# Performance work log

Measured on AMD Instinct MI355X. Metric: run time of the kernel, lower is better.

## Reference

```python
import jax, jax.numpy as jnp
import numpy as np

# ---- dims from init_kwargs ----
CB, DB = 2, 256
IN_DIM = CB + DB            # control_bits + data_bits
OUT_UNITS = DB              # output_units = data_bits
STATE_UNITS = 512           # hidden_state_dim
NUM_HEADS = 2
NUM_SHIFT = 3
M = 64                      # memory content size (word length)
B, S = 16, 512
N_ADDR = S                  # memory_addresses_size == -1 -> seq_len

# per-head interface parameter layout: shift(s), jd, jump(3), gamma, erase, add, key, beta, gate
SPLITS = [NUM_SHIFT, 1, 3, 1, M, M, M, 1, 1]
OFFS = np.cumsum([0] + SPLITS).tolist()
UPD_PER_HEAD = OFFS[-1]
READ_SIZE = NUM_HEADS * M
UPDATE_SIZE = NUM_HEADS * UPD_PER_HEAD
CTRL_IN = IN_DIM + STATE_UNITS + READ_SIZE
EPS = 1e-12


def setup_inputs() -> dict:
    key = jax.random.key(0)
    ks = jax.random.split(key, 4)
    sc = 1.0 / np.sqrt(CTRL_IN)
    return {
        "inputs": jax.random.normal(ks[0], (B, S, IN_DIM), jnp.float32),
        "W_s": jax.random.normal(ks[1], (CTRL_IN, STATE_UNITS), jnp.float32) * sc,
        "b_s": jnp.zeros((STATE_UNITS,), jnp.float32),
        "W_o": jax.random.normal(ks[2], (CTRL_IN, OUT_UNITS), jnp.float32) * sc,
        "b_o": jnp.zeros((OUT_UNITS,), jnp.float32),
        "W_u": jax.random.normal(ks[3], (CTRL_IN, UPDATE_SIZE), jnp.float32) * sc,
        "b_u": jnp.zeros((UPDATE_SIZE,), jnp.float32),
    }


def _cell(carry, x_t, W_s, b_s, W_o, b_o, W_u, b_u):
    state, wt, wt_dyn, mem = carry          # [B,St], [B,H,N], [B,H,N], [B,M,N]
    # --- read from memory with previous head attention ---
    read = jnp.einsum('bhn,bmn->bhm', wt, mem).reshape(B, READ_SIZE)
    # --- controller (single-layer RNN producing output / state / interface params) ---
    comb = jnp.concatenate([x_t, state, read], axis=-1)
    new_state = jax.nn.sigmoid(comb @ W_s + b_s)
    out = jax.nn.sigmoid(comb @ W_o + b_o)
    upd = (comb @ W_u + b_u).reshape(B, NUM_HEADS, UPD_PER_HEAD)
    s_raw, jd, j, gamma, erase, add, k, beta, g = [
        upd[..., OFFS[i]:OFFS[i + 1]] for i in range(len(SPLITS))]
    s = jax.nn.softmax(jax.nn.softplus(s_raw), axis=-1)     # [B,H,SHIFT]
    jd = jax.nn.sigmoid(jd)                                 # [B,H,1]
    j = jax.nn.softmax(j, axis=-1)                          # [B,H,3]
    gamma = 1.0 + jax.nn.softplus(gamma)                    # [B,H,1]
    erase = jax.nn.sigmoid(erase)                           # [B,H,M]
    beta = jax.nn.softplus(beta)                            # [B,H,1]
    g = jax.nn.sigmoid(g)                                   # [B,H,1]
    # --- bookmark (dynamic snapshot) update ---
    wt_dyn_new = (1.0 - jd) * wt_dyn + jd * wt
    wt_fixed = jnp.zeros((1, 1, N_ADDR), mem.dtype).at[..., 0].set(1.0)
    # --- jump between current head / dynamic bookmark / fixed address 0 ---
    w = j[..., 0:1] * wt + j[..., 1:2] * wt_dyn_new + j[..., 2:3] * wt_fixed
    # --- content addressing (is_cam=True): cosine sim key vs memory columns ---
    kn = k / (jnp.linalg.norm(k, axis=-1, keepdims=True) + EPS)
    mn = mem / (jnp.linalg.norm(mem, axis=1, keepdims=True) + EPS)
    wt_k = jax.nn.softmax(beta * jnp.einsum('bhm,bmn->bhn', kn, mn), axis=-1)
    w = g * wt_k + (1.0 - g) * w
    # --- circular shift convolution (small fixed kernel) ---
    half = NUM_SHIFT // 2
    w = sum(s[..., i:i + 1] * jnp.roll(w, i - half, axis=-1) for i in range(NUM_SHIFT))
    # --- sharpening ---
    w = w ** gamma
    w = w / (jnp.sum(w, axis=-1, keepdims=True) + EPS)
    # --- memory update: erase then add (outer products summed over heads) ---
    mem = mem * (1.0 - jnp.einsum('bhm,bhn->bmn', erase, w))
    mem = mem + jnp.einsum('bhm,bhn->bmn', add, w)
    return (new_state, w, wt_dyn_new, mem), out


def reference(inputs, W_s, b_s, W_o, b_o, W_u, b_u):
    state0 = jnp.ones((B, STATE_UNITS), inputs.dtype)
    wt0 = jnp.zeros((B, NUM_HEADS, N_ADDR), inputs.dtype).at[..., 0].set(1.0)
    mem0 = jnp.full((B, M, N_ADDR), 0.01, inputs.dtype)
    def step(c, x):
        return _cell(c, x, W_s, b_s, W_o, b_o, W_u, b_u)
    _, ys = jax.lax.scan(step, (state0, wt0, wt0, mem0), jnp.swapaxes(inputs, 0, 1))
    return jnp.swapaxes(ys, 0, 1)  # [B, S, OUT_UNITS]
```

## Files before the change

kernel.cpp:

```cpp
#include <hip/hip_runtime.h>
#include <math.h>

#define B_    16
#define S_    512
#define IN_   258
#define ST_   512
#define RD_   128
#define M_    64
#define N_    512
#define H_    2
#define UPD_  404
#define UPH_  202
#define COLS_ 916
#define CPAD_ 920
#define G_MM  10
#define CPB_  92
#define ROLES_ 11

#define XPART_F  (8192*CPAD_)
#define STATE_F  (B_*513*ST_)
#define READ_F   (B_*513*RD_)
#define UPDB_F   (2*B_*408)
#define NFLAGS_  (2*B_*S_ + B_*513)

#define AT_LD(p)    __hip_atomic_load((p), __ATOMIC_RELAXED, __HIP_MEMORY_SCOPE_AGENT)
#define AT_ST(p,v)  __hip_atomic_store((p), (v), __ATOMIC_RELAXED, __HIP_MEMORY_SCOPE_AGENT)
#define AT_ADD(p)   __hip_atomic_fetch_add((p), 1, __ATOMIC_RELAXED, __HIP_MEMORY_SCOPE_AGENT)

struct SmemMM {
  float comb[640];
  float part[5][CPB_];
};
struct SmemMB {
  float mem[64*513];
  float wt[2][512];
  float dyn[2][512];
  float wscr[2][512];
  float upd[408];
  float kn[2][64];
  float es[2][64];
  float ad[2][64];
  float rpart[2*8*64];
  float red[16];
  float smalls[24];
};

__device__ __forceinline__ float sigm(float x){ return 1.f/(1.f+__expf(-x)); }
__device__ __forceinline__ float splus(float x){ return fmaxf(x,0.f)+log1pf(__expf(-fabsf(x))); }

__device__ __forceinline__ void redMax2(float&a,float&b,float* red,int tid){
  #pragma unroll
  for(int o=32;o;o>>=1){ a=fmaxf(a,__shfl_xor(a,o)); b=fmaxf(b,__shfl_xor(b,o)); }
  if((tid&63)==0){ red[(tid>>6)*2]=a; red[(tid>>6)*2+1]=b; }
  __syncthreads();
  a=red[0]; b=red[1];
  #pragma unroll
  for(int i=1;i<8;i++){ a=fmaxf(a,red[2*i]); b=fmaxf(b,red[2*i+1]); }
  __syncthreads();
}
__device__ __forceinline__ void redSum2(float&a,float&b,float* red,int tid){
  #pragma unroll
  for(int o=32;o;o>>=1){ a+=__shfl_xor(a,o); b+=__shfl_xor(b,o); }
  if((tid&63)==0){ red[(tid>>6)*2]=a; red[(tid>>6)*2+1]=b; }
  __syncthreads();
  a=red[0]; b=red[1];
  #pragma unroll
  for(int i=1;i<8;i++){ a+=red[2*i]; b+=red[2*i+1]; }
  __syncthreads();
}

__device__ __forceinline__ void spinCnt(const int* p, int target){
  int c=0;
  while(AT_LD(p) < target){
    __builtin_amdgcn_s_sleep(1);
    if(++c > (1<<22)) break;
  }
}

__device__ __forceinline__ void p2_step(SmemMB& S, int bb, int tnext,
    float* __restrict__ readSeq, int* __restrict__ go, int tid)
{
  const int m=tid&63, g=tid>>6;
  float e0=S.es[0][m], e1=S.es[1][m], a0=S.ad[0][m], a1=S.ad[1][m];
  float r0=0.f, r1=0.f;
  const int base=m*513;
  #pragma unroll 4
  for(int kk=0;kk<64;kk++){
    int n=g*64+kk;
    float w0=S.wt[0][n], w1=S.wt[1][n];
    float v=S.mem[base+n];
    float E=fmaf(e0,w0,e1*w1);
    float A=fmaf(a0,w0,a1*w1);
    v=fmaf(v,-E,v)+A;
    S.mem[base+n]=v;
    r0=fmaf(w0,v,r0);
    r1=fmaf(w1,v,r1);
  }
  S.rpart[(0*8+g)*64+m]=r0;
  S.rpart[(1*8+g)*64+m]=r1;
  __syncthreads();
  if(tid<128){
    int h=tid>>6, mm=tid&63;
    float s=0.f;
    #pragma unroll
    for(int gg=0;gg<8;gg++) s+=S.rpart[(h*8+gg)*64+mm];
    AT_ST(&readSeq[(size_t)(bb*513+tnext)*RD_+tid], s);
  }
  __syncthreads();
  if(tid==0)
    AT_ST(&go[bb*513+tnext], 1);
}

__global__ void init_kernel(float* __restrict__ stateSeq, int* __restrict__ flags, int nflags)
{
  int i = blockIdx.x*blockDim.x + threadIdx.x;
  if (i < nflags) flags[i] = 0;
  if (i < B_*ST_) { int b = i>>9, c = i&511; stateSeq[(size_t)(b*513)*ST_ + c] = 1.f; }
}

__global__ __launch_bounds__(256) void xpart_kernel(const float* __restrict__ X,
    const float* __restrict__ Ws, const float* __restrict__ Wu,
    const float* __restrict__ bs, const float* __restrict__ bu,
    float* __restrict__ xpart)
{
  __shared__ float Xs[32][65];
  __shared__ float Wsh[32][65];
  const int row0=blockIdx.x*64, c0=blockIdx.y*64;
  const int tid=threadIdx.x, tx=tid&15, ty=tid>>4;
  float acc[4][4]={};
  for(int k0=0;k0<IN_;k0+=32){
    for(int i=tid;i<32*64;i+=256){
      int kk=i&31, tt=i>>5, k=k0+kk;
      Xs[kk][tt]=(k<IN_)?X[(size_t)(row0+tt)*IN_+k]:0.f;
    }
    for(int i=tid;i<32*64;i+=256){
      int cc=i&63, kk=i>>6, k=k0+kk, c=c0+cc;
      float v=0.f;
      if(k<IN_){
        if(c<512) v=Ws[(size_t)k*512+c];
        else if(c<COLS_) v=Wu[(size_t)k*404+(c-512)];
      }
      Wsh[kk][cc]=v;
    }
    __syncthreads();
    #pragma unroll
    for(int kk=0;kk<32;kk++){
      float xv[4],wv[4];
      #pragma unroll
      for(int i=0;i<4;i++) xv[i]=Xs[kk][ty*4+i];
      #pragma unroll
      for(int j=0;j<4;j++) wv[j]=Wsh[kk][tx*4+j];
      #pragma unroll
      for(int i=0;i<4;i++)
        #pragma unroll
        for(int j=0;j<4;j++) acc[i][j]=fmaf(xv[i],wv[j],acc[i][j]);
    }
    __syncthreads();
  }
  #pragma unroll
  for(int i=0;i<4;i++){
    int r=row0+ty*4+i;
    #pragma unroll
    for(int j=0;j<4;j++){
      int c=c0+tx*4+j;
      if(c<COLS_){
        float bias=(c<512)?bs[c]:bu[c-512];
        xpart[(size_t)r*CPAD_+c]=acc[i][j]+bias;
      }
    }
  }
}

__global__ __launch_bounds__(256) void outgemm_kernel(const float* __restrict__ X,
    const float* __restrict__ stateSeq, const float* __restrict__ readSeq,
    const float* __restrict__ Wo, const float* __restrict__ bo, float* __restrict__ out)
{
  __shared__ float Cs[32][65];
  __shared__ float Wsh[32][65];
  const int row0=blockIdx.x*64, c0=blockIdx.y*64;
  const int tid=threadIdx.x, tx=tid&15, ty=tid>>4;
  float acc[4][4]={};
  for(int k0=0;k0<898;k0+=32){
    for(int i=tid;i<32*64;i+=256){
      int kk=i&31, tt=i>>5, k=k0+kk, row=row0+tt;
      float v=0.f;
      if(k<258) v=X[(size_t)row*IN_+k];
      else if(k<770){ int b=row>>9,t=row&511; v=stateSeq[(size_t)(b*513+t)*ST_+(k-258)]; }
      else if(k<898){ int b=row>>9,t=row&511; v=readSeq[(size_t)(b*513+t)*RD_+(k-770)]; }
      Cs[kk][tt]=v;
    }
    for(int i=tid;i<32*64;i+=256){
      int cc=i&63, kk=i>>6, k=k0+kk;
      Wsh[kk][cc]=(k<898)?Wo[(size_t)k*256+(c0+cc)]:0.f;
    }
    __syncthreads();
    #pragma unroll
    for(int kk=0;kk<32;kk++){
      float xv[4],wv[4];
      #pragma unroll
      for(int i=0;i<4;i++) xv[i]=Cs[kk][ty*4+i];
      #pragma unroll
      for(int j=0;j<4;j++) wv[j]=Wsh[kk][tx*4+j];
      #pragma unroll
      for(int i=0;i<4;i++)
        #pragma unroll
        for(int j=0;j<4;j++) acc[i][j]=fmaf(xv[i],wv[j],acc[i][j]);
    }
    __syncthreads();
  }
  #pragma unroll
  for(int i=0;i<4;i++){
    int r=row0+ty*4+i;
    #pragma unroll
    for(int j=0;j<4;j++){
      int c=c0+tx*4+j;
      out[(size_t)r*256+c]=sigm(acc[i][j]+bo[c]);
    }
  }
}

__global__ __launch_bounds__(512, 2) void main_kernel(
    const float* __restrict__ Ws, const float* __restrict__ Wu,
    const float* __restrict__ xpart, float* __restrict__ stateSeq,
    float* __restrict__ readSeq, float* __restrict__ updBuf,
    int* __restrict__ arriveS, int* __restrict__ arriveU, int* __restrict__ go)
{
  extern __shared__ char smem[];
  const int bb   = blockIdx.x & 15;
  const int role = blockIdx.x >> 4;
  const int tid  = threadIdx.x;

  if (role < G_MM) {
    SmemMM& S = *(SmemMM*)smem;
    const int c  = tid % CPB_;
    const int rc = tid / CPB_;
    const int cg = role*CPB_ + c;
    const bool cvalid = (cg < COLS_);
    const float* Wp; int ldw, ci;
    if (cg < 512) { Wp = Ws; ldw = 512; ci = cg; }
    else          { Wp = Wu; ldw = 404; ci = cvalid ? (cg-512) : 0; }
    float wreg[128];
    if (rc < 5) {
      #pragma unroll
      for (int j = 0; j < 128; ++j)
        wreg[j] = Wp[(size_t)(258 + rc*128 + j)*ldw + ci];
    }
    for (int t = 0; t < S_; ++t) {
      float xp = 0.f;
      if (tid < CPB_ && cvalid) xp = xpart[(size_t)(bb*512 + t)*CPAD_ + cg];
      if (t > 0) {
        if (tid == 0) spinCnt(&arriveS[bb*S_ + (t-1)], 6);
        __syncthreads();
      }
      if (tid < 128)
        ((float4*)S.comb)[tid] = ((const float4*)&stateSeq[(size_t)(bb*513 + t)*ST_])[tid];
      __syncthreads();
      float acc = 0.f;
      if (rc < 4) {
        const float4* cb = (const float4*)&S.comb[rc*128];
        #pragma unroll
        for (int j4 = 0; j4 < 32; ++j4) {
          float4 cv = cb[j4];
          acc = fmaf(cv.x, wreg[4*j4+0], acc);
          acc = fmaf(cv.y, wreg[4*j4+1], acc);
          acc = fmaf(cv.z, wreg[4*j4+2], acc);
          acc = fmaf(cv.w, wreg[4*j4+3], acc);
        }
      }
      if (tid == 0) spinCnt(&go[bb*513 + t], 1);
      __syncthreads();
      if (tid < 32)
        ((float4*)&S.comb[512])[tid] = ((const float4*)&readSeq[(size_t)(bb*513 + t)*RD_])[tid];
      __syncthreads();
      if (rc == 4) {
        const float4* cb = (const float4*)&S.comb[512];
        #pragma unroll
        for (int j4 = 0; j4 < 32; ++j4) {
          float4 cv = cb[j4];
          acc = fmaf(cv.x, wreg[4*j4+0], acc);
          acc = fmaf(cv.y, wreg[4*j4+1], acc);
          acc = fmaf(cv.z, wreg[4*j4+2], acc);
          acc = fmaf(cv.w, wreg[4*j4+3], acc);
        }
      }
      if (rc < 5) S.part[rc][c] = acc;
      __syncthreads();
      if (tid < CPB_ && cvalid) {
        float pre = xp + S.part[0][c] + S.part[1][c] + S.part[2][c]
                       + S.part[3][c] + S.part[4][c];
        if (cg < 512)
          AT_ST(&stateSeq[(size_t)(bb*513 + t + 1)*ST_ + cg], sigm(pre));
        else
          AT_ST(&updBuf[(size_t)((t&1)*B_ + bb)*408 + (cg - 512)], pre);
      }
      __syncthreads();
      if (tid == 0) {
        if (role <= 5) AT_ADD(&arriveS[bb*S_ + t]);
        if (role >= 5) AT_ADD(&arriveU[bb*S_ + t]);
      }
    }
  } else {
    SmemMB& S = *(SmemMB*)smem;
    for (int i = tid; i < 64*513; i += 512) S.mem[i] = 0.01f;
    {
      float o0 = (tid == 0) ? 1.f : 0.f;
      S.wt[0][tid]=o0; S.wt[1][tid]=o0; S.dyn[0][tid]=o0; S.dyn[1][tid]=o0;
    }
    if (tid < 128) { S.es[tid>>6][tid&63]=0.f; S.ad[tid>>6][tid&63]=0.f; }
    __syncthreads();
    p2_step(S, bb, 0, readSeq, go, tid);

    for (int t = 0; t < S_-1; ++t) {
      if (tid == 0) spinCnt(&arriveU[bb*S_ + t], 5);
      __syncthreads();
      {
        const unsigned long long* up8 =
            (const unsigned long long*)&updBuf[(size_t)((t&1)*B_ + bb)*408];
        if (tid < 202) {
          unsigned long long v = __hip_atomic_load(&up8[tid], __ATOMIC_RELAXED,
                                                   __HIP_MEMORY_SCOPE_AGENT);
          union { unsigned long long u; float f[2]; } cv; cv.u = v;
          S.upd[2*tid]   = cv.f[0];
          S.upd[2*tid+1] = cv.f[1];
        }
      }
      __syncthreads();
      if (tid < 128) {
        int h=tid>>6, m=tid&63; const float* u=&S.upd[h*UPH_];
        S.es[h][m]=sigm(u[8+m]);
        S.ad[h][m]=u[72+m];
        float kv=u[136+m];
        float s2=kv*kv;
        #pragma unroll
        for(int o=32;o;o>>=1) s2+=__shfl_xor(s2,o);
        if(m==0) S.smalls[20+h]=1.f/(sqrtf(s2)+1e-12f);
      } else if (tid < 130) {
        int h = tid-128; const float* u = &S.upd[h*UPH_];
        float sp0=splus(u[0]), sp1=splus(u[1]), sp2=splus(u[2]);
        float mx=fmaxf(sp0,fmaxf(sp1,sp2));
        float e0=__expf(sp0-mx), e1=__expf(sp1-mx), e2=__expf(sp2-mx);
        float inv=1.f/(e0+e1+e2);
        S.smalls[h*3+0]=e0*inv; S.smalls[h*3+1]=e1*inv; S.smalls[h*3+2]=e2*inv;
        float j0=u[4], j1=u[5], j2=u[6];
        float mj=fmaxf(j0,fmaxf(j1,j2));
        float f0=__expf(j0-mj), f1=__expf(j1-mj), f2=__expf(j2-mj);
        float invj=1.f/(f0+f1+f2);
        S.smalls[6+h*3+0]=f0*invj; S.smalls[6+h*3+1]=f1*invj; S.smalls[6+h*3+2]=f2*invj;
        S.smalls[12+h]=sigm(u[3]);
        S.smalls[14+h]=1.f+splus(u[7]);
        S.smalls[16+h]=splus(u[200]);
        S.smalls[18+h]=sigm(u[201]);
      }
      __syncthreads();
      if (tid < 128) {
        int h=tid>>6, m=tid&63;
        S.kn[h][m]=S.upd[h*UPH_+136+m]*S.smalls[20+h];
      }
      __syncthreads();
      {
        int n = tid;
        float nrm=0.f, d0=0.f, d1=0.f;
        #pragma unroll 8
        for (int m=0;m<64;m++){
          float v=S.mem[m*513+n];
          nrm=fmaf(v,v,nrm);
          d0=fmaf(S.kn[0][m],v,d0);
          d1=fmaf(S.kn[1][m],v,d1);
        }
        float inv=1.f/(sqrtf(nrm)+1e-12f);
        float sc0=S.smalls[16]*d0*inv, sc1=S.smalls[17]*d1*inv;
        float mx0=sc0, mx1=sc1; redMax2(mx0,mx1,S.red,tid);
        float ex0=__expf(sc0-mx0), ex1=__expf(sc1-mx1);
        float sm0=ex0, sm1=ex1; redSum2(sm0,sm1,S.red,tid);
        float wtk0=ex0/sm0, wtk1=ex1/sm1;
        float jd0=S.smalls[12], jd1=S.smalls[13];
        float g0=S.smalls[18],  g1=S.smalls[19];
        float w0o=S.wt[0][n], w1o=S.wt[1][n];
        float dn0=fmaf(jd0, w0o - S.dyn[0][n], S.dyn[0][n]);
        float dn1=fmaf(jd1, w1o - S.dyn[1][n], S.dyn[1][n]);
        S.dyn[0][n]=dn0; S.dyn[1][n]=dn1;
        float fx=(n==0)?1.f:0.f;
        float wm0=S.smalls[6+0]*w0o + S.smalls[6+1]*dn0 + S.smalls[6+2]*fx;
        float wm1=S.smalls[9+0]*w1o + S.smalls[9+1]*dn1 + S.smalls[9+2]*fx;
        float wc0=fmaf(g0, wtk0-wm0, wm0);
        float wc1=fmaf(g1, wtk1-wm1, wm1);
        S.wscr[0][n]=wc0; S.wscr[1][n]=wc1;
        __syncthreads();
        int np=(n+1)&511, nm=(n-1)&511;
        float wsh0=S.smalls[0]*S.wscr[0][np]+S.smalls[1]*S.wscr[0][n]+S.smalls[2]*S.wscr[0][nm];
        float wsh1=S.smalls[3]*S.wscr[1][np]+S.smalls[4]*S.wscr[1][n]+S.smalls[5]*S.wscr[1][nm];
        float gam0=S.smalls[14], gam1=S.smalls[15];
        float wp0=(wsh0>0.f)?__expf(gam0*__logf(wsh0)):0.f;
        float wp1=(wsh1>0.f)?__expf(gam1*__logf(wsh1)):0.f;
        float ds0=wp0, ds1=wp1; redSum2(ds0,ds1,S.red,tid);
        S.wt[0][n]=wp0/(ds0+1e-12f);
        S.wt[1][n]=wp1/(ds1+1e-12f);
      }
      __syncthreads();
      p2_step(S, bb, t+1, readSeq, go, tid);
    }
  }
}

extern "C" void kernel_launch(void* const* d_in, const int* in_sizes, int n_in,
                              void* d_out, int out_size, void* d_ws, size_t ws_size,
                              hipStream_t stream) {
  (void)in_sizes; (void)n_in; (void)out_size;
  const float* X  = (const float*)d_in[0];
  const float* Ws = (const float*)d_in[1];
  const float* bs = (const float*)d_in[2];
  const float* Wo = (const float*)d_in[3];
  const float* bo = (const float*)d_in[4];
  const float* Wu = (const float*)d_in[5];
  const float* bu = (const float*)d_in[6];
  float* out = (float*)d_out;

  const size_t needed = (size_t)(XPART_F + STATE_F + READ_F + UPDB_F)*4 + (size_t)NFLAGS_*4;
  if (ws_size < needed) return;

  float* xpart    = (float*)d_ws;
  float* stateSeq = xpart + XPART_F;
  float* readSeq  = stateSeq + STATE_F;
  float* updBuf   = readSeq + READ_F;
  int*   flags    = (int*)(updBuf + UPDB_F);
  int*   arriveS  = flags;
  int*   arriveU  = flags + B_*S_;
  int*   go       = flags + 2*B_*S_;

  hipLaunchKernelGGL(init_kernel, dim3((NFLAGS_ + 255)/256), dim3(256), 0, stream,
                     stateSeq, flags, NFLAGS_);
  hipLaunchKernelGGL(xpart_kernel, dim3(128, 15), dim3(256), 0, stream, X, Ws, Wu, bs, bu, xpart);

  (void)hipFuncSetAttribute((const void*)main_kernel,
        hipFuncAttributeMaxDynamicSharedMemorySize, (int)sizeof(SmemMB));
  void* kargs[] = { (void*)&Ws, (void*)&Wu, (void*)&xpart, (void*)&stateSeq,
                    (void*)&readSeq, (void*)&updBuf, (void*)&arriveS, (void*)&arriveU,
                    (void*)&go };
  hipLaunchCooperativeKernel((const void*)main_kernel, dim3(B_*ROLES_), dim3(512),
                             kargs, (unsigned)sizeof(SmemMB), stream);

  hipLaunchKernelGGL(outgemm_kernel, dim3(128, 4), dim3(256), 0, stream,
                     X, stateSeq, readSeq, Wo, bo, out);
}
```

Baseline: 6.842 ms.

## Move read-vector contribution of update params into memory block to shorten critical path

Update-parameter blocks no longer wait for the memory block's read vector. They compute only the input and state parts of the matmul, and the memory block adds the read·W_u term itself from register-cached weights. This removes one cross-block handoff (waiting on go, then reloading the read vector) from the serial chain of each step. Columns are also rebalanced into 6 state roles and 4 update roles, and the column-norm computation moves off the key-scoring loop to just after the memory update. The cost is higher register pressure in the memory block (128 weights per thread) and extra work on that block's critical path.

```diff
diff --git a/kernel.cpp b/kernel.cpp
--- a/kernel.cpp
+++ b/kernel.cpp
@@ -6,15 +6,14 @@
 #define IN_   258
 #define ST_   512
 #define RD_   128
-#define M_    64
-#define N_    512
-#define H_    2
 #define UPD_  404
 #define UPH_  202
 #define COLS_ 916
 #define CPAD_ 920
-#define G_MM  10
-#define CPB_  92
+#define SROLES 6
+#define UROLES 4
+#define SCPB  86
+#define UCPB  101
 #define ROLES_ 11
 
 #define XPART_F  (8192*CPAD_)
@@ -29,7 +28,7 @@
 
 struct SmemMM {
   float comb[640];
-  float part[5][CPB_];
+  float part[5][UCPB];
 };
 struct SmemMB {
   float mem[64*513];
@@ -41,8 +40,9 @@
   float es[2][64];
   float ad[2][64];
   float rpart[2*8*64];
+  float readv[128];
   float red[16];
-  float smalls[24];
+  float smalls[20];
 };
 
 __device__ __forceinline__ float sigm(float x){ return 1.f/(1.f+__expf(-x)); }
@@ -105,10 +105,18 @@
     #pragma unroll
     for(int gg=0;gg<8;gg++) s+=S.rpart[(h*8+gg)*64+mm];
     AT_ST(&readSeq[(size_t)(bb*513+tnext)*RD_+tid], s);
+    S.readv[tid]=s;
   }
   __syncthreads();
   if(tid==0)
     AT_ST(&go[bb*513+tnext], 1);
+}
+
+__device__ __forceinline__ float colNormInv(const SmemMB& S, int tid){
+  float nrm=0.f;
+  #pragma unroll 8
+  for(int m=0;m<64;m++){ float v=S.mem[m*513+tid]; nrm=fmaf(v,v,nrm); }
+  return 1.f/(sqrtf(nrm)+1e-12f);
 }
 
 __global__ void init_kernel(float* __restrict__ stateSeq, int* __restrict__ flags, int nflags)
@@ -230,26 +238,29 @@
   const int role = blockIdx.x >> 4;
   const int tid  = threadIdx.x;
 
-  if (role < G_MM) {
+  if (role < SROLES + UROLES) {
     SmemMM& S = *(SmemMM*)smem;
-    const int c  = tid % CPB_;
-    const int rc = tid / CPB_;
-    const int cg = role*CPB_ + c;
-    const bool cvalid = (cg < COLS_);
+    const bool isState = (role < SROLES);
+    const int CPB = isState ? SCPB : UCPB;
+    const int NCH = isState ? 5 : 4;
+    const int c  = tid % CPB;
+    const int rc = tid / CPB;
+    const int cg = isState ? (role*SCPB + c) : (512 + (role-SROLES)*UCPB + c);
+    const bool cvalid = (cg < (isState ? 512 : COLS_));
     const float* Wp; int ldw, ci;
-    if (cg < 512) { Wp = Ws; ldw = 512; ci = cg; }
-    else          { Wp = Wu; ldw = 404; ci = cvalid ? (cg-512) : 0; }
+    if (isState) { Wp = Ws; ldw = 512; ci = cvalid ? cg : 0; }
+    else         { Wp = Wu; ldw = 404; ci = cg - 512; }
     float wreg[128];
-    if (rc < 5) {
+    if (rc < NCH) {
       #pragma unroll
       for (int j = 0; j < 128; ++j)
         wreg[j] = Wp[(size_t)(258 + rc*128 + j)*ldw + ci];
     }
     for (int t = 0; t < S_; ++t) {
       float xp = 0.f;
-      if (tid < CPB_ && cvalid) xp = xpart[(size_t)(bb*512 + t)*CPAD_ + cg];
+      if (tid < CPB && cvalid) xp = xpart[(size_t)(bb*512 + t)*CPAD_ + cg];
       if (t > 0) {
-        if (tid == 0) spinCnt(&arriveS[bb*S_ + (t-1)], 6);
+        if (tid == 0) spinCnt(&arriveS[bb*S_ + (t-1)], SROLES);
         __syncthreads();
       }
       if (tid < 128)
@@ -267,40 +278,49 @@
           acc = fmaf(cv.w, wreg[4*j4+3], acc);
         }
       }
-      if (tid == 0) spinCnt(&go[bb*513 + t], 1);
-      __syncthreads();
-      if (tid < 32)
-        ((float4*)&S.comb[512])[tid] = ((const float4*)&readSeq[(size_t)(bb*513 + t)*RD_])[tid];
-      __syncthreads();
-      if (rc == 4) {
-        const float4* cb = (const float4*)&S.comb[512];
-        #pragma unroll
-        for (int j4 = 0; j4 < 32; ++j4) {
-          float4 cv = cb[j4];
-          acc = fmaf(cv.x, wreg[4*j4+0], acc);
-          acc = fmaf(cv.y, wreg[4*j4+1], acc);
-          acc = fmaf(cv.z, wreg[4*j4+2], acc);
-          acc = fmaf(cv.w, wreg[4*j4+3], acc);
+      if (isState) {
+        if (tid == 0) spinCnt(&go[bb*513 + t], 1);
+        __syncthreads();
+        if (tid < 32)
+          ((float4*)&S.comb[512])[tid] = ((const float4*)&readSeq[(size_t)(bb*513 + t)*RD_])[tid];
+        __syncthreads();
+        if (rc == 4) {
+          const float4* cb = (const float4*)&S.comb[512];
+          #pragma unroll
+          for (int j4 = 0; j4 < 32; ++j4) {
+            float4 cv = cb[j4];
+            acc = fmaf(cv.x, wreg[4*j4+0], acc);
+            acc = fmaf(cv.y, wreg[4*j4+1], acc);
+            acc = fmaf(cv.z, wreg[4*j4+2], acc);
+            acc = fmaf(cv.w, wreg[4*j4+3], acc);
+          }
         }
       }
-      if (rc < 5) S.part[rc][c] = acc;
-      __syncthreads();
-      if (tid < CPB_ && cvalid) {
-        float pre = xp + S.part[0][c] + S.part[1][c] + S.part[2][c]
-                       + S.part[3][c] + S.part[4][c];
-        if (cg < 512)
+      if (rc < NCH) S.part[rc][c] = acc;
+      __syncthreads();
+      if (tid < CPB && cvalid) {
+        float pre = xp + S.part[0][c] + S.part[1][c] + S.part[2][c] + S.part[3][c];
+        if (isState) {
+          pre += S.part[4][c];
           AT_ST(&stateSeq[(size_t)(bb*513 + t + 1)*ST_ + cg], sigm(pre));
-        else
+        } else {
           AT_ST(&updBuf[(size_t)((t&1)*B_ + bb)*408 + (cg - 512)], pre);
+        }
       }
       __syncthreads();
       if (tid == 0) {
-        if (role <= 5) AT_ADD(&arriveS[bb*S_ + t]);
-        if (role >= 5) AT_ADD(&arriveU[bb*S_ + t]);
+        if (isState) AT_ADD(&arriveS[bb*S_ + t]);
+        else         AT_ADD(&arriveU[bb*S_ + t]);
       }
     }
   } else {
     SmemMB& S = *(SmemMB*)smem;
+    float wcol[128];
+    if (tid < UPD_) {
+      #pragma unroll
+      for (int j = 0; j < 128; ++j)
+        wcol[j] = Wu[(size_t)(770 + j)*404 + tid];
+    }
     for (int i = tid; i < 64*513; i += 512) S.mem[i] = 0.01f;
     {
       float o0 = (tid == 0) ? 1.f : 0.f;
@@ -309,20 +329,17 @@
     if (tid < 128) { S.es[tid>>6][tid&63]=0.f; S.ad[tid>>6][tid&63]=0.f; }
     __syncthreads();
     p2_step(S, bb, 0, readSeq, go, tid);
+    float nrmInv = colNormInv(S, tid);
 
     for (int t = 0; t < S_-1; ++t) {
-      if (tid == 0) spinCnt(&arriveU[bb*S_ + t], 5);
-      __syncthreads();
-      {
-        const unsigned long long* up8 =
-            (const unsigned long long*)&updBuf[(size_t)((t&1)*B_ + bb)*408];
-        if (tid < 202) {
-          unsigned long long v = __hip_atomic_load(&up8[tid], __ATOMIC_RELAXED,
-                                                   __HIP_MEMORY_SCOPE_AGENT);
-          union { unsigned long long u; float f[2]; } cv; cv.u = v;
-          S.upd[2*tid]   = cv.f[0];
-          S.upd[2*tid+1] = cv.f[1];
-        }
+      if (tid == 0) spinCnt(&arriveU[bb*S_ + t], UROLES);
+      __syncthreads();
+      if (tid < UPD_) {
+        float updv = AT_LD(&updBuf[(size_t)((t&1)*B_ + bb)*408 + tid]);
+        float rd = 0.f;
+        #pragma unroll
+        for (int j = 0; j < 128; ++j) rd = fmaf(wcol[j], S.readv[j], rd);
+        S.upd[tid] = updv + rd;
       }
       __syncthreads();
       if (tid < 128) {
@@ -333,7 +350,7 @@
         float s2=kv*kv;
         #pragma unroll
         for(int o=32;o;o>>=1) s2+=__shfl_xor(s2,o);
-        if(m==0) S.smalls[20+h]=1.f/(sqrtf(s2)+1e-12f);
+        S.kn[h][m]=kv*(1.f/(sqrtf(s2)+1e-12f));
       } else if (tid < 130) {
         int h = tid-128; const float* u = &S.upd[h*UPH_];
         float sp0=splus(u[0]), sp1=splus(u[1]), sp2=splus(u[2]);
@@ -352,23 +369,16 @@
         S.smalls[18+h]=sigm(u[201]);
       }
       __syncthreads();
-      if (tid < 128) {
-        int h=tid>>6, m=tid&63;
-        S.kn[h][m]=S.upd[h*UPH_+136+m]*S.smalls[20+h];
-      }
-      __syncthreads();
       {
         int n = tid;
-        float nrm=0.f, d0=0.f, d1=0.f;
+        float d0=0.f, d1=0.f;
         #pragma unroll 8
         for (int m=0;m<64;m++){
           float v=S.mem[m*513+n];
-          nrm=fmaf(v,v,nrm);
           d0=fmaf(S.kn[0][m],v,d0);
           d1=fmaf(S.kn[1][m],v,d1);
         }
-        float inv=1.f/(sqrtf(nrm)+1e-12f);
-        float sc0=S.smalls[16]*d0*inv, sc1=S.smalls[17]*d1*inv;
+        float sc0=S.smalls[16]*d0*nrmInv, sc1=S.smalls[17]*d1*nrmInv;
         float mx0=sc0, mx1=sc1; redMax2(mx0,mx1,S.red,tid);
         float ex0=__expf(sc0-mx0), ex1=__expf(sc1-mx1);
         float sm0=ex0, sm1=ex1; redSum2(sm0,sm1,S.red,tid);
@@ -398,6 +408,7 @@
       }
       __syncthreads();
       p2_step(S, bb, t+1, readSeq, go, tid);
+      nrmInv = colNormInv(S, tid);
     }
   }
 }
```

Measured after the change: 8.202 ms. 19.9% more time.

## Replace counter flags with per-element value/tag packed 64-bit handoffs

Applied to the files above, without the earlier changes.

Inter-block communication no longer uses arrival counters and go flags. Each state, read and update value is stored as a 64-bit word holding the value and a timestep tag, and consumers poll each element until the tag matches. This drops the extra barriers and the single-thread spin-then-sync round trips. The memory column norms are also computed right after the memory update rather than inside the key-similarity loop, and the key normalisation is folded into one pass. In exchange it doubles workspace traffic for the sequences, has many threads polling global memory, and makes the outgemm read 64-bit tagged values.

```diff
diff --git a/kernel.cpp b/kernel.cpp
--- a/kernel.cpp
+++ b/kernel.cpp
@@ -6,9 +6,6 @@
 #define IN_   258
 #define ST_   512
 #define RD_   128
-#define M_    64
-#define N_    512
-#define H_    2
 #define UPD_  404
 #define UPH_  202
 #define COLS_ 916
@@ -17,15 +14,33 @@
 #define CPB_  92
 #define ROLES_ 11
 
+typedef unsigned long long u64t;
+
 #define XPART_F  (8192*CPAD_)
-#define STATE_F  (B_*513*ST_)
-#define READ_F   (B_*513*RD_)
-#define UPDB_F   (2*B_*408)
-#define NFLAGS_  (2*B_*S_ + B_*513)
-
-#define AT_LD(p)    __hip_atomic_load((p), __ATOMIC_RELAXED, __HIP_MEMORY_SCOPE_AGENT)
-#define AT_ST(p,v)  __hip_atomic_store((p), (v), __ATOMIC_RELAXED, __HIP_MEMORY_SCOPE_AGENT)
-#define AT_ADD(p)   __hip_atomic_fetch_add((p), 1, __ATOMIC_RELAXED, __HIP_MEMORY_SCOPE_AGENT)
+#define STTAG_N  ((size_t)B_*513*512)
+#define RDTAG_N  ((size_t)B_*513*128)
+#define UPTAG_N  ((size_t)B_*2*512)
+#define TAGS_N   (STTAG_N + RDTAG_N + UPTAG_N)
+
+#define AT_LD64(p)   __hip_atomic_load((p), __ATOMIC_RELAXED, __HIP_MEMORY_SCOPE_AGENT)
+#define AT_ST64(p,v) __hip_atomic_store((p), (v), __ATOMIC_RELAXED, __HIP_MEMORY_SCOPE_AGENT)
+
+union VT { u64t u; struct { float v; int t; } s; };
+__device__ __forceinline__ u64t packVT(float v, int t){ VT x; x.s.v=v; x.s.t=t; return x.u; }
+__device__ __forceinline__ float vtVal(u64t u){ VT x; x.u=u; return x.s.v; }
+__device__ __forceinline__ int   vtTag(u64t u){ VT x; x.u=u; return x.s.t; }
+__host__ __device__ __forceinline__ float vtValH(u64t u){ VT x; x.u=u; return x.s.v; }
+
+__device__ __forceinline__ float pollVal(const u64t* p, int want){
+  u64t v = AT_LD64(p);
+  int c=0;
+  while (vtTag(v) != want){
+    __builtin_amdgcn_s_sleep(1);
+    v = AT_LD64(p);
+    if (++c > (1<<22)) break;
+  }
+  return vtVal(v);
+}
 
 struct SmemMM {
   float comb[640];
@@ -42,7 +57,7 @@
   float ad[2][64];
   float rpart[2*8*64];
   float red[16];
-  float smalls[24];
+  float smalls[20];
 };
 
 __device__ __forceinline__ float sigm(float x){ return 1.f/(1.f+__expf(-x)); }
@@ -69,16 +84,8 @@
   __syncthreads();
 }
 
-__device__ __forceinline__ void spinCnt(const int* p, int target){
-  int c=0;
-  while(AT_LD(p) < target){
-    __builtin_amdgcn_s_sleep(1);
-    if(++c > (1<<22)) break;
-  }
-}
-
 __device__ __forceinline__ void p2_step(SmemMB& S, int bb, int tnext,
-    float* __restrict__ readSeq, int* __restrict__ go, int tid)
+    u64t* __restrict__ rdTag, int tid)
 {
   const int m=tid&63, g=tid>>6;
   float e0=S.es[0][m], e1=S.es[1][m], a0=S.ad[0][m], a1=S.ad[1][m];
@@ -104,18 +111,31 @@
     float s=0.f;
     #pragma unroll
     for(int gg=0;gg<8;gg++) s+=S.rpart[(h*8+gg)*64+mm];
-    AT_ST(&readSeq[(size_t)(bb*513+tnext)*RD_+tid], s);
-  }
-  __syncthreads();
-  if(tid==0)
-    AT_ST(&go[bb*513+tnext], 1);
-}
-
-__global__ void init_kernel(float* __restrict__ stateSeq, int* __restrict__ flags, int nflags)
+    AT_ST64(&rdTag[((size_t)(bb*513+tnext))*RD_+tid], packVT(s, tnext+1));
+  }
+  __syncthreads();
+}
+
+__device__ __forceinline__ float colNormInv(const SmemMB& S, int tid){
+  float nrm=0.f;
+  #pragma unroll 8
+  for(int m=0;m<64;m++){ float v=S.mem[m*513+tid]; nrm=fmaf(v,v,nrm); }
+  return 1.f/(sqrtf(nrm)+1e-12f);
+}
+
+__global__ void init_kernel(u64t* __restrict__ stTag, u64t* __restrict__ rdTag,
+                            u64t* __restrict__ upTag)
 {
-  int i = blockIdx.x*blockDim.x + threadIdx.x;
-  if (i < nflags) flags[i] = 0;
-  if (i < B_*ST_) { int b = i>>9, c = i&511; stateSeq[(size_t)(b*513)*ST_ + c] = 1.f; }
+  size_t i = (size_t)blockIdx.x*blockDim.x + threadIdx.x;
+  if (i < STTAG_N) {
+    size_t rem = i % (513*512);
+    int t = (int)(rem >> 9);
+    stTag[i] = (t==0) ? packVT(1.f, 1) : 0ULL;
+  } else if (i < STTAG_N + RDTAG_N) {
+    rdTag[i - STTAG_N] = 0ULL;
+  } else if (i < TAGS_N) {
+    upTag[i - STTAG_N - RDTAG_N] = 0ULL;
+  }
 }
 
 __global__ __launch_bounds__(256) void xpart_kernel(const float* __restrict__ X,
@@ -172,7 +192,7 @@
 }
 
 __global__ __launch_bounds__(256) void outgemm_kernel(const float* __restrict__ X,
-    const float* __restrict__ stateSeq, const float* __restrict__ readSeq,
+    const u64t* __restrict__ stTag, const u64t* __restrict__ rdTag,
     const float* __restrict__ Wo, const float* __restrict__ bo, float* __restrict__ out)
 {
   __shared__ float Cs[32][65];
@@ -185,8 +205,8 @@
       int kk=i&31, tt=i>>5, k=k0+kk, row=row0+tt;
       float v=0.f;
       if(k<258) v=X[(size_t)row*IN_+k];
-      else if(k<770){ int b=row>>9,t=row&511; v=stateSeq[(size_t)(b*513+t)*ST_+(k-258)]; }
-      else if(k<898){ int b=row>>9,t=row&511; v=readSeq[(size_t)(b*513+t)*RD_+(k-770)]; }
+      else if(k<770){ int b=row>>9,t=row&511; v=vtValH(stTag[((size_t)(b*513+t))*512+(k-258)]); }
+      else if(k<898){ int b=row>>9,t=row&511; v=vtValH(rdTag[((size_t)(b*513+t))*128+(k-770)]); }
       Cs[kk][tt]=v;
     }
     for(int i=tid;i<32*64;i+=256){
@@ -221,9 +241,8 @@
 
 __global__ __launch_bounds__(512, 2) void main_kernel(
     const float* __restrict__ Ws, const float* __restrict__ Wu,
-    const float* __restrict__ xpart, float* __restrict__ stateSeq,
-    float* __restrict__ readSeq, float* __restrict__ updBuf,
-    int* __restrict__ arriveS, int* __restrict__ arriveU, int* __restrict__ go)
+    const float* __restrict__ xpart, u64t* __restrict__ stTag,
+    u64t* __restrict__ rdTag, u64t* __restrict__ upTag)
 {
   extern __shared__ char smem[];
   const int bb   = blockIdx.x & 15;
@@ -248,12 +267,7 @@
     for (int t = 0; t < S_; ++t) {
       float xp = 0.f;
       if (tid < CPB_ && cvalid) xp = xpart[(size_t)(bb*512 + t)*CPAD_ + cg];
-      if (t > 0) {
-        if (tid == 0) spinCnt(&arriveS[bb*S_ + (t-1)], 6);
-        __syncthreads();
-      }
-      if (tid < 128)
-        ((float4*)S.comb)[tid] = ((const float4*)&stateSeq[(size_t)(bb*513 + t)*ST_])[tid];
+      S.comb[tid] = pollVal(&stTag[((size_t)(bb*513 + t))*512 + tid], t+1);
       __syncthreads();
       float acc = 0.f;
       if (rc < 4) {
@@ -267,10 +281,8 @@
           acc = fmaf(cv.w, wreg[4*j4+3], acc);
         }
       }
-      if (tid == 0) spinCnt(&go[bb*513 + t], 1);
-      __syncthreads();
-      if (tid < 32)
-        ((float4*)&S.comb[512])[tid] = ((const float4*)&readSeq[(size_t)(bb*513 + t)*RD_])[tid];
+      if (tid < RD_)
+        S.comb[512 + tid] = pollVal(&rdTag[((size_t)(bb*513 + t))*RD_ + tid], t+1);
       __syncthreads();
       if (rc == 4) {
         const float4* cb = (const float4*)&S.comb[512];
@@ -289,14 +301,9 @@
         float pre = xp + S.part[0][c] + S.part[1][c] + S.part[2][c]
                        + S.part[3][c] + S.part[4][c];
         if (cg < 512)
-          AT_ST(&stateSeq[(size_t)(bb*513 + t + 1)*ST_ + cg], sigm(pre));
+          AT_ST64(&stTag[((size_t)(bb*513 + t + 1))*512 + cg], packVT(sigm(pre), t+2));
         else
-          AT_ST(&updBuf[(size_t)((t&1)*B_ + bb)*408 + (cg - 512)], pre);
-      }
-      __syncthreads();
-      if (tid == 0) {
-        if (role <= 5) AT_ADD(&arriveS[bb*S_ + t]);
-        if (role >= 5) AT_ADD(&arriveU[bb*S_ + t]);
+          AT_ST64(&upTag[((size_t)(bb*2 + (t&1)))*512 + (cg-512)], packVT(pre, t+1));
       }
     }
   } else {
@@ -308,22 +315,12 @@
     }
     if (tid < 128) { S.es[tid>>6][tid&63]=0.f; S.ad[tid>>6][tid&63]=0.f; }
     __syncthreads();
-    p2_step(S, bb, 0, readSeq, go, tid);
+    p2_step(S, bb, 0, rdTag, tid);
+    float nrmInv = colNormInv(S, tid);
 
     for (int t = 0; t < S_-1; ++t) {
-      if (tid == 0) spinCnt(&arriveU[bb*S_ + t], 5);
-      __syncthreads();
-      {
-        const unsigned long long* up8 =
-            (const unsigned long long*)&updBuf[(size_t)((t&1)*B_ + bb)*408];
-        if (tid < 202) {
-          unsigned long long v = __hip_atomic_load(&up8[tid], __ATOMIC_RELAXED,
-                                                   __HIP_MEMORY_SCOPE_AGENT);
-          union { unsigned long long u; float f[2]; } cv; cv.u = v;
-          S.upd[2*tid]   = cv.f[0];
-          S.upd[2*tid+1] = cv.f[1];
-        }
-      }
+      if (tid < UPD_)
+        S.upd[tid] = pollVal(&upTag[((size_t)(bb*2 + (t&1)))*512 + tid], t+1);
       __syncthreads();
       if (tid < 128) {
         int h=tid>>6, m=tid&63; const float* u=&S.upd[h*UPH_];
@@ -333,7 +330,7 @@
         float s2=kv*kv;
         #pragma unroll
         for(int o=32;o;o>>=1) s2+=__shfl_xor(s2,o);
-        if(m==0) S.smalls[20+h]=1.f/(sqrtf(s2)+1e-12f);
+        S.kn[h][m]=kv*(1.f/(sqrtf(s2)+1e-12f));
       } else if (tid < 130) {
         int h = tid-128; const float* u = &S.upd[h*UPH_];
         float sp0=splus(u[0]), sp1=splus(u[1]), sp2=splus(u[2]);
@@ -352,23 +349,16 @@
         S.smalls[18+h]=sigm(u[201]);
       }
       __syncthreads();
-      if (tid < 128) {
-        int h=tid>>6, m=tid&63;
-        S.kn[h][m]=S.upd[h*UPH_+136+m]*S.smalls[20+h];
-      }
-      __syncthreads();
       {
         int n = tid;
-        float nrm=0.f, d0=0.f, d1=0.f;
+        float d0=0.f, d1=0.f;
         #pragma unroll 8
         for (int m=0;m<64;m++){
           float v=S.mem[m*513+n];
-          nrm=fmaf(v,v,nrm);
           d0=fmaf(S.kn[0][m],v,d0);
           d1=fmaf(S.kn[1][m],v,d1);
         }
-        float inv=1.f/(sqrtf(nrm)+1e-12f);
-        float sc0=S.smalls[16]*d0*inv, sc1=S.smalls[17]*d1*inv;
+        float sc0=S.smalls[16]*d0*nrmInv, sc1=S.smalls[17]*d1*nrmInv;
         float mx0=sc0, mx1=sc1; redMax2(mx0,mx1,S.red,tid);
         float ex0=__expf(sc0-mx0), ex1=__expf(sc1-mx1);
         float sm0=ex0, sm1=ex1; redSum2(sm0,sm1,S.red,tid);
@@ -397,7 +387,8 @@
         S.wt[1][n]=wp1/(ds1+1e-12f);
       }
       __syncthreads();
-      p2_step(S, bb, t+1, readSeq, go, tid);
+      p2_step(S, bb, t+1, rdTag, tid);
+      nrmInv = colNormInv(S, tid);
     }
   }
 }
@@ -415,30 +406,25 @@
   const float* bu = (const float*)d_in[6];
   float* out = (float*)d_out;
 
-  const size_t needed = (size_t)(XPART_F + STATE_F + READ_F + UPDB_F)*4 + (size_t)NFLAGS_*4;
+  const size_t needed = (size_t)XPART_F*4 + TAGS_N*8;
   if (ws_size < needed) return;
 
-  float* xpart    = (float*)d_ws;
-  float* stateSeq = xpart + XPART_F;
-  float* readSeq  = stateSeq + STATE_F;
-  float* updBuf   = readSeq + READ_F;
-  int*   flags    = (int*)(updBuf + UPDB_F);
-  int*   arriveS  = flags;
-  int*   arriveU  = flags + B_*S_;
-  int*   go       = flags + 2*B_*S_;
-
-  hipLaunchKernelGGL(init_kernel, dim3((NFLAGS_ + 255)/256), dim3(256), 0, stream,
-                     stateSeq, flags, NFLAGS_);
+  float* xpart  = (float*)d_ws;
+  u64t*  stTag  = (u64t*)(xpart + XPART_F);
+  u64t*  rdTag  = stTag + STTAG_N;
+  u64t*  upTag  = rdTag + RDTAG_N;
+
+  hipLaunchKernelGGL(init_kernel, dim3((unsigned)((TAGS_N + 255)/256)), dim3(256), 0, stream,
+                     stTag, rdTag, upTag);
   hipLaunchKernelGGL(xpart_kernel, dim3(128, 15), dim3(256), 0, stream, X, Ws, Wu, bs, bu, xpart);
 
   (void)hipFuncSetAttribute((const void*)main_kernel,
         hipFuncAttributeMaxDynamicSharedMemorySize, (int)sizeof(SmemMB));
-  void* kargs[] = { (void*)&Ws, (void*)&Wu, (void*)&xpart, (void*)&stateSeq,
-                    (void*)&readSeq, (void*)&updBuf, (void*)&arriveS, (void*)&arriveU,
-                    (void*)&go };
+  void* kargs[] = { (void*)&Ws, (void*)&Wu, (void*)&xpart, (void*)&stTag,
+                    (void*)&rdTag, (void*)&upTag };
   hipLaunchCooperativeKernel((const void*)main_kernel, dim3(B_*ROLES_), dim3(512),
                              kargs, (unsigned)sizeof(SmemMB), stream);
 
   hipLaunchKernelGGL(outgemm_kernel, dim3(128, 4), dim3(256), 0, stream,
-                     X, stateSeq, readSeq, Wo, bo, out);
-}
+                     X, stTag, rdTag, Wo, bo, out);
+}
```

After: 6.179 ms. 1.11x faster.
